# Kernel optimization log

Measured on AMD Instinct MI355X. Metric: run time of the kernel, lower is better.

## Reference

```python
import jax, jax.numpy as jnp
import numpy as np

N_HEAD = 12
TOP_M = 16
MIN_SIZE = 2
MAX_SIZE = 8
ALPHA = 1.0
EPS = 1e-6

# Note: in the torch source, minimize_det=True and minimize_det=False select the
# identical subset (the sign flip in the score is exactly undone by flipping the
# comparisons), so we implement the single equivalent rule: maximize
# s = -log(det(K_S K_S^T) + 1e-6) / |S|**alpha.

def _token(qi, i, k_all, v_all):
    """Greedy DPP subset selection for one query token i. qi:[d], k_all/v_all:[T,d]."""
    T, d = k_all.shape
    slots = jnp.arange(MAX_SIZE)
    sim = k_all @ qi
    sim = jnp.where(jnp.arange(T) <= i, sim, -jnp.inf)  # causal mask
    vals, topidx = jax.lax.top_k(sim, TOP_M)
    avail0 = jnp.isfinite(vals) & (topidx != i)  # i is removed from candidates
    k_cand = k_all[topidx]                        # [M,d]
    cand_norm = jnp.sum(k_cand * k_cand, axis=-1)  # [M]
    ki = k_all[i]
    sel0 = jnp.zeros((MAX_SIZE,), jnp.int32).at[0].set(i.astype(jnp.int32))
    s0 = jax.lax.stop_gradient(-jnp.log(jnp.dot(ki, ki) + EPS))  # |S|=1 => size^alpha=1

    def body(state, _):
        sel, count, cur_s, avail, done = state
        # E: selected key vectors in slots < count, zeros elsewhere
        E = jnp.where((slots < count)[:, None], k_all[sel], 0.0)  # [S,d]
        G0 = E @ E.T                                              # [S,S]
        cross = k_cand @ E.T  # [M,S]; column `count` is 0 since that E row is 0
        u = (slots == count).astype(E.dtype)  # one-hot insertion slot
        # Gram of S u {c} for every candidate c, identity-padded beyond slot count
        grams = (G0[None]
                 + u[None, :, None] * cross[:, None, :]
                 + cross[:, :, None] * u[None, None, :]
                 + cand_norm[:, None, None] * (u[:, None] * u[None, :])[None])
        grams = grams + jnp.diag(jnp.where(slots > count, 1.0, 0.0))[None]
        det = jnp.linalg.det(grams.astype(jnp.float32))  # [M]
        s = -jnp.log(det + EPS) / (count + 1).astype(jnp.float32) ** ALPHA
        s = jax.lax.stop_gradient(jnp.where(avail, s, -jnp.inf))
        best = jnp.argmax(s)
        best_s = s[best]
        accept = (~done) & jnp.any(avail) & ((best_s > cur_s) | (count < MIN_SIZE))
        sel = jnp.where(accept & (slots == count), topidx[best].astype(jnp.int32), sel)
        avail = avail & ~(accept & (jnp.arange(TOP_M) == best))
        cur_s = jnp.where(accept, best_s, cur_s)
        count = count + accept.astype(count.dtype)
        done = done | ~accept
        return (sel, count, cur_s, avail, done), None

    init = (sel0, jnp.int32(1), s0, avail0, jnp.bool_(False))
    (sel, count, _, _, _), _ = jax.lax.scan(body, init, None, length=MAX_SIZE - 1)
    w = (slots < count).astype(v_all.dtype)
    return (v_all[sel] * w[:, None]).sum(0) / count.astype(v_all.dtype)

_tokens = jax.vmap(_token, in_axes=(0, 0, None, None))  # over T

def _head(qh, kh, vh):
    return _tokens(qh, jnp.arange(qh.shape[0]), kh, vh)

_attn = jax.vmap(jax.vmap(_head))  # over B, H

def _forward(x, W_attn, b_attn, W_proj, b_proj):
    B, T, C = x.shape
    hs = C // N_HEAD
    qkv = x @ W_attn + b_attn
    q, k, v = jnp.split(qkv, 3, axis=-1)
    q = q.reshape(B, T, N_HEAD, hs).transpose(0, 2, 1, 3)
    k = k.reshape(B, T, N_HEAD, hs).transpose(0, 2, 1, 3)
    v = v.reshape(B, T, N_HEAD, hs).transpose(0, 2, 1, 3)
    y = _attn(q, k, v)  # [B,H,T,hs]
    y = y.transpose(0, 2, 1, 3).reshape(B, T, C)
    return y @ W_proj + b_proj  # dropout=0.0 (eval)

def setup_inputs():
    key = jax.random.key(0)
    ks = jax.random.split(key, 3)
    B, T, C = 4, 512, 768
    return {
        "x": jax.random.normal(ks[0], (B, T, C), jnp.float32),
        "W_attn": jax.random.normal(ks[1], (C, 3 * C), jnp.float32) * 0.02,
        "b_attn": jnp.zeros((3 * C,), jnp.float32),
        "W_proj": jax.random.normal(ks[2], (C, C), jnp.float32) * 0.02,
        "b_proj": jnp.zeros((C,), jnp.float32),
    }

def reference(x, W_attn, b_attn, W_proj, b_proj):
    return _forward(x, W_attn, b_attn, W_proj, b_proj)
```

## Files before the change

### kernel.cpp

```cpp
#include <hip/hip_runtime.h>
#include <math.h>

constexpr int Bc = 4, Tc = 512, Cc = 768, Hc = 12, HSc = 64;
constexpr int QKVN = 3 * Cc;
constexpr double EPSd = 1e-6;

typedef unsigned short u16;
typedef __attribute__((ext_vector_type(8))) short short8;
typedef __attribute__((ext_vector_type(4))) float f32x4;

__device__ __forceinline__ u16 f2bf(float x) {
  unsigned u = __float_as_uint(x);
  return (u16)((u + 0x7FFFu + ((u >> 16) & 1u)) >> 16);
}
__device__ __forceinline__ float bf2f(u16 h) {
  return __uint_as_float((unsigned)h << 16);
}

__device__ __forceinline__ void gload16(const u16* g, u16* l) {
  __builtin_amdgcn_global_load_lds(
      (const __attribute__((address_space(1))) void*)g,
      (__attribute__((address_space(3))) void*)l, 16, 0, 0);
}

__global__ void __launch_bounds__(256) convsplit3(
    const float* __restrict__ in, u16* __restrict__ H, u16* __restrict__ M,
    u16* __restrict__ L) {
  const int i = blockIdx.x * 256 + threadIdx.x;
  const float4 v = ((const float4*)in)[i];
  const float x[4] = {v.x, v.y, v.z, v.w};
  ushort4 hv, mv, lv;
  u16* hp = (u16*)&hv; u16* mp = (u16*)&mv; u16* lp = (u16*)&lv;
#pragma unroll
  for (int c = 0; c < 4; ++c) {
    const u16 h = f2bf(x[c]);
    const float r1 = x[c] - bf2f(h);
    const u16 m = f2bf(r1);
    const u16 l = f2bf(r1 - bf2f(m));
    hp[c] = h; mp[c] = m; lp[c] = l;
  }
  ((ushort4*)H)[i] = hv;
  ((ushort4*)M)[i] = mv;
  ((ushort4*)L)[i] = lv;
}

__global__ void __launch_bounds__(256) convsplit3_t(
    const float* __restrict__ W, u16* __restrict__ Th, u16* __restrict__ Tm,
    u16* __restrict__ Tl, int K, int Nn) {
  __shared__ float t[64][65];
  const int k0 = blockIdx.x * 64, n0 = blockIdx.y * 64;
#pragma unroll
  for (int u = 0; u < 16; ++u) {
    const int idx = u * 256 + threadIdx.x;
    const int r = idx >> 6, c = idx & 63;
    t[r][c] = W[(size_t)(k0 + r) * Nn + n0 + c];
  }
  __syncthreads();
#pragma unroll
  for (int u = 0; u < 16; ++u) {
    const int idx = u * 256 + threadIdx.x;
    const int n = idx >> 6, k = idx & 63;
    const float x = t[k][n];
    const u16 h = f2bf(x);
    const float r1 = x - bf2f(h);
    const u16 m = f2bf(r1);
    const u16 l = f2bf(r1 - bf2f(m));
    Th[(size_t)(n0 + n) * K + k0 + k] = h;
    Tm[(size_t)(n0 + n) * K + k0 + k] = m;
    Tl[(size_t)(n0 + n) * K + k0 + k] = l;
  }
}

template <bool WRITE_PARTIAL>
__global__ void __launch_bounds__(128, 2) gemm_mfma3(
    const u16* __restrict__ A, const u16* __restrict__ B,
    const float* __restrict__ bias, float* __restrict__ outp,
    int N, int kPerSplit, int strideA, int strideB) {
  __shared__ __align__(16) u16 AsF[3 * 64 * 32];
  __shared__ __align__(16) u16 BsF[3 * 128 * 32];
  const int tid = threadIdx.x;
  const int wid = tid >> 6;
  const int lane = tid & 63;
  const int lm = lane & 15, kg = lane >> 4;
  const int rb = blockIdx.x * 64;
  const int cb = blockIdx.y * 128;
  const int kBeg = blockIdx.z * kPerSplit;

  const int trow = tid >> 2;
  const int tc4 = tid & 3;
  const int krot = ((tc4 - (trow >> 1)) & 3) * 8;
  const int sLds = tid * 8;
  int aOff = (rb + trow) * 768 + kBeg + krot;
  int bOff = (cb + trow) * 768 + kBeg + krot;

  f32x4 acc[4][4];
#pragma unroll
  for (int mf = 0; mf < 4; ++mf)
#pragma unroll
    for (int nf = 0; nf < 4; ++nf) acc[mf][nf] = (f32x4){0.f, 0.f, 0.f, 0.f};

  const int nIter = kPerSplit / 32;
  const int ckA = ((kg + (lm >> 1)) & 3) * 8;

  for (int it = 0; it < nIter; ++it) {
    __syncthreads();
#pragma unroll
    for (int v = 0; v < 12; ++v)
      gload16(B + (size_t)(v >> 2) * strideB + (v & 3) * (32 * 768) + bOff,
              &BsF[(v >> 2) * 4096 + (v & 3) * 1024 + sLds]);
#pragma unroll
    for (int u = 0; u < 6; ++u)
      gload16(A + (size_t)(u >> 1) * strideA + (u & 1) * (32 * 768) + aOff,
              &AsF[(u >> 1) * 2048 + (u & 1) * 1024 + sLds]);
    aOff += 32; bOff += 32;
    __syncthreads();
    short8 ah[4], am[4], al[4];
#pragma unroll
    for (int mf = 0; mf < 4; ++mf) {
      const int ro = (mf * 16 + lm) * 32 + ckA;
      ah[mf] = *(const short8*)&AsF[ro];
      am[mf] = *(const short8*)&AsF[2048 + ro];
      al[mf] = *(const short8*)&AsF[4096 + ro];
    }
#pragma unroll
    for (int nf = 0; nf < 4; ++nf) {
      const int co = (wid * 64 + nf * 16 + lm) * 32 + ckA;
      const short8 bh = *(const short8*)&BsF[co];
      const short8 bm = *(const short8*)&BsF[4096 + co];
      const short8 bl = *(const short8*)&BsF[8192 + co];
#pragma unroll
      for (int mf = 0; mf < 4; ++mf) {
        acc[mf][nf] = __builtin_amdgcn_mfma_f32_16x16x32_bf16(
            al[mf], bh, acc[mf][nf], 0, 0, 0);
        acc[mf][nf] = __builtin_amdgcn_mfma_f32_16x16x32_bf16(
            ah[mf], bl, acc[mf][nf], 0, 0, 0);
        acc[mf][nf] = __builtin_amdgcn_mfma_f32_16x16x32_bf16(
            am[mf], bm, acc[mf][nf], 0, 0, 0);
        acc[mf][nf] = __builtin_amdgcn_mfma_f32_16x16x32_bf16(
            am[mf], bh, acc[mf][nf], 0, 0, 0);
        acc[mf][nf] = __builtin_amdgcn_mfma_f32_16x16x32_bf16(
            ah[mf], bm, acc[mf][nf], 0, 0, 0);
        acc[mf][nf] = __builtin_amdgcn_mfma_f32_16x16x32_bf16(
            ah[mf], bh, acc[mf][nf], 0, 0, 0);
      }
    }
  }

  const int colb = cb + wid * 64 + lm;
  if (WRITE_PARTIAL) {
    float* Pp = outp + (size_t)blockIdx.z * 2048 * N;
#pragma unroll
    for (int mf = 0; mf < 4; ++mf)
#pragma unroll
      for (int r2 = 0; r2 < 4; ++r2) {
        float* orow = Pp + (size_t)(rb + mf * 16 + kg * 4 + r2) * N + colb;
        orow[0]  = acc[mf][0][r2];
        orow[16] = acc[mf][1][r2];
        orow[32] = acc[mf][2][r2];
        orow[48] = acc[mf][3][r2];
      }
  } else {
    const float bb0 = bias[colb], bb1 = bias[colb + 16];
    const float bb2 = bias[colb + 32], bb3 = bias[colb + 48];
#pragma unroll
    for (int mf = 0; mf < 4; ++mf)
#pragma unroll
      for (int r2 = 0; r2 < 4; ++r2) {
        float* orow = outp + (size_t)(rb + mf * 16 + kg * 4 + r2) * N + colb;
        orow[0]  = acc[mf][0][r2] + bb0;
        orow[16] = acc[mf][1][r2] + bb1;
        orow[32] = acc[mf][2][r2] + bb2;
        orow[48] = acc[mf][3][r2] + bb3;
      }
  }
}

__global__ void __launch_bounds__(256) reduce_bias_kernel(
    const float* __restrict__ P, const float* __restrict__ bias,
    float* __restrict__ outp, int MN, int N, int KS) {
  const int idx4 = (blockIdx.x * 256 + threadIdx.x) * 4;
  float4 acc = *(const float4*)&P[idx4];
  for (int ks = 1; ks < KS; ++ks) {
    const float4 p = *(const float4*)&P[(size_t)ks * MN + idx4];
    acc.x += p.x; acc.y += p.y; acc.z += p.z; acc.w += p.w;
  }
  const int col = idx4 % N;
  const float4 b4 = *(const float4*)&bias[col];
  acc.x += b4.x; acc.y += b4.y; acc.z += b4.z; acc.w += b4.w;
  *(float4*)&outp[idx4] = acc;
}

__global__ void __launch_bounds__(256) sims_kernel(
    const float* __restrict__ qkv, float* __restrict__ S) {
  const int bh = blockIdx.y;
  const int b = bh / Hc, h = bh % Hc;
  int it = 0;
  {
    const int t = blockIdx.x;
    while ((it + 1) * (it + 2) / 2 <= t) ++it;
  }
  const int jt = blockIdx.x - it * (it + 1) / 2;
  const int tid = threadIdx.x;
  const int tx = tid & 15, ty = tid >> 4;
  __shared__ float Qs[HSc][68];
  __shared__ float Ks[HSc][68];
  const float* base = qkv + (size_t)b * Tc * QKVN + h * HSc;
  {
    const int row = tid >> 2;
    const int d0 = (tid & 3) * 16;
    const float* qrow = base + (size_t)(it * 64 + row) * QKVN;
    const float* krow = base + (size_t)(jt * 64 + row) * QKVN + Cc;
#pragma unroll
    for (int u = 0; u < 4; ++u) {
      const float4 q4 = *(const float4*)&qrow[d0 + u * 4];
      const float4 k4 = *(const float4*)&krow[d0 + u * 4];
      Qs[d0 + u * 4 + 0][row] = q4.x; Qs[d0 + u * 4 + 1][row] = q4.y;
      Qs[d0 + u * 4 + 2][row] = q4.z; Qs[d0 + u * 4 + 3][row] = q4.w;
      Ks[d0 + u * 4 + 0][row] = k4.x; Ks[d0 + u * 4 + 1][row] = k4.y;
      Ks[d0 + u * 4 + 2][row] = k4.z; Ks[d0 + u * 4 + 3][row] = k4.w;
    }
  }
  __syncthreads();
  float acc[4][4];
#pragma unroll
  for (int m = 0; m < 4; ++m)
#pragma unroll
    for (int n = 0; n < 4; ++n) acc[m][n] = 0.0f;
#pragma unroll 4
  for (int d = 0; d < HSc; ++d) {
    const float4 a4 = *(const float4*)&Qs[d][ty * 4];
    const float4 b4 = *(const float4*)&Ks[d][tx * 4];
    const float a[4] = {a4.x, a4.y, a4.z, a4.w};
    const float bv[4] = {b4.x, b4.y, b4.z, b4.w};
#pragma unroll
    for (int m = 0; m < 4; ++m)
#pragma unroll
      for (int n = 0; n < 4; ++n) acc[m][n] += a[m] * bv[n];
  }
  float* Shead = S + (size_t)bh * Tc * Tc;
#pragma unroll
  for (int m = 0; m < 4; ++m) {
    const int i = it * 64 + ty * 4 + m;
    float4 o4 = {acc[m][0], acc[m][1], acc[m][2], acc[m][3]};
    *(float4*)&Shead[(size_t)i * Tc + jt * 64 + tx * 4] = o4;
  }
}

__global__ void __launch_bounds__(256) topk_kernel(
    const float* __restrict__ S, int* __restrict__ topidx,
    unsigned* __restrict__ availB) {
  const int tid = threadIdx.x;
  const int wv = tid >> 6, lane = tid & 63;
  const int tok = blockIdx.x * 4 + wv;
  const int i = tok & (Tc - 1);
  const float4* Sq = reinterpret_cast<const float4*>(S + (size_t)tok * Tc);
  unsigned long long key[8];
#pragma unroll
  for (int r = 0; r < 2; ++r) {
    const float4 v4 = Sq[lane * 2 + r];
    const float vv[4] = {v4.x, v4.y, v4.z, v4.w};
#pragma unroll
    for (int c = 0; c < 4; ++c) {
      const int j = lane * 8 + r * 4 + c;
      const unsigned u = __float_as_uint(vv[c]);
      const unsigned s = (u & 0x80000000u) ? ~u : (u | 0x80000000u);
      key[r * 4 + c] = (j <= i)
          ? (((unsigned long long)s << 32) | (unsigned)(511 - j))
          : 0ull;
    }
  }
  unsigned avail = 0;
  for (int m = 0; m < 16; ++m) {
    unsigned long long bk = 0;
#pragma unroll
    for (int r = 0; r < 8; ++r) bk = (key[r] > bk) ? key[r] : bk;
#pragma unroll
    for (int msk = 1; msk <= 32; msk <<= 1) {
      const unsigned long long ok = __shfl_xor(bk, msk);
      bk = (ok > bk) ? ok : bk;
    }
    const int j = 511 - (int)(unsigned)(bk & 0xFFFFFFFFull);
    const unsigned shi = (unsigned)(bk >> 32);
    if (lane == 0) topidx[(size_t)tok * 16 + m] = j & 511;
    if (shi > 0x007FFFFFu && j != i) avail |= (1u << m);
#pragma unroll
    for (int r = 0; r < 8; ++r) key[r] = (key[r] == bk) ? 0ull : key[r];
  }
  if (lane == 0) availB[tok] = avail;
}

__global__ void __launch_bounds__(256, 4) select_kernel(
    const float* __restrict__ qkv, const int* __restrict__ topidx,
    const unsigned* __restrict__ availB, u16* __restrict__ yh,
    u16* __restrict__ ym, u16* __restrict__ yl) {
  const int tid = threadIdx.x;
  const int wv = tid >> 6, lane = tid & 63;
  const int half = lane >> 5;
  const int l32 = lane & 31;
  const int m = l32 >> 1;
  const int q = l32 & 1;
  const int hbase = half << 5;

  const int tok = blockIdx.x * 8 + wv * 2 + half;
  const int bh = tok >> 9;
  const int i = tok & (Tc - 1);
  const int b = bh / Hc;
  const int h = bh % Hc;

  const float* base = qkv + (size_t)b * Tc * QKVN + h * HSc;
  const float* kbase = base + Cc;
  const float* vbase = base + 2 * Cc;

  const int tidx = topidx[(size_t)tok * 16 + m];
  unsigned avail = availB[tok];

  float kreg[32], kireg[32];
  {
    const float* kc = kbase + (size_t)tidx * QKVN + q * 32;
    const float* ki = kbase + (size_t)i * QKVN + q * 32;
#pragma unroll
    for (int u = 0; u < 8; ++u) {
      const float4 c4 = *(const float4*)&kc[u * 4];
      const float4 i4 = *(const float4*)&ki[u * 4];
      kreg[u * 4 + 0] = c4.x; kreg[u * 4 + 1] = c4.y;
      kreg[u * 4 + 2] = c4.z; kreg[u * 4 + 3] = c4.w;
      kireg[u * 4 + 0] = i4.x; kireg[u * 4 + 1] = i4.y;
      kireg[u * 4 + 2] = i4.z; kireg[u * 4 + 3] = i4.w;
    }
  }
  float cnorm_f = 0.0f, c0_f = 0.0f, kii_f = 0.0f;
#pragma unroll
  for (int e = 0; e < 32; ++e) {
    cnorm_f += kreg[e] * kreg[e];
    c0_f += kreg[e] * kireg[e];
    kii_f += kireg[e] * kireg[e];
  }
  cnorm_f += __shfl_xor(cnorm_f, 1);
  c0_f += __shfl_xor(c0_f, 1);
  kii_f += __shfl_xor(kii_f, 1);

  const double kii = (double)kii_f;
  double z[8];
#pragma unroll
  for (int t = 0; t < 8; ++t) z[t] = 0.0;
  z[0] = (double)c0_f / sqrt(kii);
  double schur = (double)cnorm_f - z[0] * z[0];
  double detS = kii;
  double Dprev = 0.0;
  int count = 1;
  int sel[8];
  sel[0] = i;
#pragma unroll
  for (int a = 1; a < 8; ++a) sel[a] = 0;
  bool hdone = false;

#pragma unroll
  for (int it = 0; it < 7; ++it) {
    const double D = detS * schur + EPSd;
    const bool act = ((avail >> m) & 1u) != 0;
    const bool bad = !(D > 0.0);
    double dkey = act ? (bad ? -INFINITY : D) : INFINITY;
    int bm = m;
#pragma unroll
    for (int msk = 2; msk <= 16; msk <<= 1) {
      const double ok2 = __shfl_xor(dkey, msk);
      const int om = __shfl_xor(bm, msk);
      const bool t2 = (ok2 < dkey) || (ok2 == dkey && om < bm);
      dkey = t2 ? ok2 : dkey;
      bm = t2 ? om : bm;
    }
    const double Dbest = __shfl(D, hbase | (bm * 2));
    bool acc_ok;
    if (it == 0) {
      acc_ok = true;
    } else {
      double pA = Dbest, pB = Dprev;
#pragma unroll
      for (int j = 0; j < it; ++j) pA *= Dbest;
#pragma unroll
      for (int j = 0; j < it + 1; ++j) pB *= Dprev;
      acc_ok = ((avail >> bm) & 1u) && (Dbest >= 0.0) && (Dprev >= 0.0) &&
               (pA < pB);
    }
    const bool X = !hdone && (avail != 0u) && acc_ok;
    hdone = hdone || !X;
    if (X) {
      float cp_f = 0.0f;
#pragma unroll
      for (int e = 0; e < 32; ++e) {
        const float kb = __shfl(kreg[e], hbase | (bm * 2) | q);
        cp_f += kreg[e] * kb;
      }
      cp_f += __shfl_xor(cp_f, 1);
      const double schur_b = __shfl(schur, hbase | (bm * 2));
      double sum = 0.0;
#pragma unroll
      for (int t = 0; t <= it; ++t) {
        const double zbt = __shfl(z[t], hbase | (bm * 2));
        sum += z[t] * zbt;
      }
      const double znew = ((double)cp_f - sum) / sqrt(schur_b);
      z[it + 1] = znew;
      schur -= znew * znew;
      detS *= schur_b;
      Dprev = Dbest;
      avail &= ~(1u << bm);
      ++count;
      sel[it + 1] = __shfl(tidx, hbase | (bm * 2));
    }
    if (__all(hdone)) break;
  }

  double acc0 = 0.0, acc1 = 0.0;
#pragma unroll
  for (int a = 0; a < 8; ++a)
    if (a < count) {
      const float* vrow = vbase + (size_t)sel[a] * QKVN;
      acc0 += (double)vrow[l32];
      acc1 += (double)vrow[l32 + 32];
    }
  const float v0 = (float)(acc0 / (double)count);
  const float v1 = (float)(acc1 / (double)count);
  const size_t yidx = (((size_t)b * Tc + i) * Hc + h) * HSc + l32;
  {
    const u16 hv = f2bf(v0);
    const float r1 = v0 - bf2f(hv);
    const u16 mv = f2bf(r1);
    yh[yidx] = hv; ym[yidx] = mv; yl[yidx] = f2bf(r1 - bf2f(mv));
  }
  {
    const u16 hv = f2bf(v1);
    const float r1 = v1 - bf2f(hv);
    const u16 mv = f2bf(r1);
    yh[yidx + 32] = hv; ym[yidx + 32] = mv;
    yl[yidx + 32] = f2bf(r1 - bf2f(mv));
  }
}

extern "C" void kernel_launch(void* const* d_in, const int* in_sizes, int n_in,
                              void* d_out, int out_size, void* d_ws, size_t ws_size,
                              hipStream_t stream) {
  (void)in_sizes; (void)n_in; (void)out_size; (void)ws_size;
  const float* x  = (const float*)d_in[0];
  const float* Wa = (const float*)d_in[1];
  const float* ba = (const float*)d_in[2];
  const float* Wp = (const float*)d_in[3];
  const float* bp = (const float*)d_in[4];
  float* out = (float*)d_out;

  constexpr size_t XPLANE = (size_t)Bc * Tc * Cc;
  constexpr size_t WAPLANE = (size_t)QKVN * Cc;
  constexpr size_t WPPLANE = (size_t)Cc * Cc;

  float* qkv = (float*)d_ws;
  int* topidx = (int*)(qkv + (size_t)Bc * Tc * QKVN);
  unsigned* availB = (unsigned*)(topidx + (size_t)Bc * Hc * Tc * 16);
  float* regionB = (float*)(availB + (size_t)Bc * Hc * Tc);
  float* S = regionB;
  float* Pproj = regionB;
  u16* Xh = (u16*)regionB;
  u16* Wath = Xh + 3 * XPLANE;
  u16* Wpth = (u16*)(regionB + (size_t)3 * 2048 * Cc);
  u16* yhp = Wpth + 3 * WPPLANE;

  const int MNproj = Bc * Tc * Cc;

  hipLaunchKernelGGL(convsplit3, dim3(1536), dim3(256), 0, stream,
                     x, Xh, Xh + XPLANE, Xh + 2 * XPLANE);
  hipLaunchKernelGGL(convsplit3_t, dim3(12, 36), dim3(256), 0, stream,
                     Wa, Wath, Wath + WAPLANE, Wath + 2 * WAPLANE, Cc, QKVN);
  hipLaunchKernelGGL((gemm_mfma3<false>), dim3(32, QKVN / 128, 1), dim3(128),
                     0, stream, Xh, Wath, ba, qkv, QKVN, Cc,
                     (int)XPLANE, (int)WAPLANE);
  hipLaunchKernelGGL(sims_kernel, dim3(36, Bc * Hc), dim3(256), 0,
                     stream, qkv, S);
  hipLaunchKernelGGL(topk_kernel, dim3(Bc * Hc * Tc / 4), dim3(256), 0,
                     stream, S, topidx, availB);
  hipLaunchKernelGGL(select_kernel, dim3(Bc * Hc * Tc / 8), dim3(256), 0,
                     stream, qkv, topidx, availB,
                     yhp, yhp + XPLANE, yhp + 2 * XPLANE);
  hipLaunchKernelGGL(convsplit3_t, dim3(12, 12), dim3(256), 0, stream,
                     Wp, Wpth, Wpth + WPPLANE, Wpth + 2 * WPPLANE, Cc, Cc);
  hipLaunchKernelGGL((gemm_mfma3<true>), dim3(32, Cc / 128, 3), dim3(128), 0,
                     stream, yhp, Wpth, nullptr, Pproj, Cc, 256,
                     (int)XPLANE, (int)WPPLANE);
  hipLaunchKernelGGL(reduce_bias_kernel, dim3(MNproj / 1024), dim3(256), 0,
                     stream, Pproj, bp, out, MNproj, Cc, 3);
}
```

Measured before the change: 288.3 us.

## Double-buffer LDS tiles in split-bf16 MFMA GEMM to overlap loads with compute

The GEMM's shared-memory A/B tiles are doubled so the next k-slice is fetched with global_load_lds while the current slice feeds the MFMA chain. This removes one of the two barriers per k-step and aims to hide global-load latency behind matrix math. LDS use per block doubles, which may limit occupancy. The loop assumes an even iteration count: with an odd count the last compute(1) would read a stale buffer.

```diff
diff --git a/kernel.cpp b/kernel.cpp
--- a/kernel.cpp
+++ b/kernel.cpp
@@ -76,8 +76,8 @@
     const u16* __restrict__ A, const u16* __restrict__ B,
     const float* __restrict__ bias, float* __restrict__ outp,
     int N, int kPerSplit, int strideA, int strideB) {
-  __shared__ __align__(16) u16 AsF[3 * 64 * 32];
-  __shared__ __align__(16) u16 BsF[3 * 128 * 32];
+  __shared__ __align__(16) u16 AsF[2][3 * 64 * 32];
+  __shared__ __align__(16) u16 BsF[2][3 * 128 * 32];
   const int tid = threadIdx.x;
   const int wid = tid >> 6;
   const int lane = tid & 63;
@@ -102,32 +102,32 @@
   const int nIter = kPerSplit / 32;
   const int ckA = ((kg + (lm >> 1)) & 3) * 8;
 
-  for (int it = 0; it < nIter; ++it) {
-    __syncthreads();
+  auto stage = [&](int buf) {
 #pragma unroll
     for (int v = 0; v < 12; ++v)
       gload16(B + (size_t)(v >> 2) * strideB + (v & 3) * (32 * 768) + bOff,
-              &BsF[(v >> 2) * 4096 + (v & 3) * 1024 + sLds]);
+              &BsF[buf][(v >> 2) * 4096 + (v & 3) * 1024 + sLds]);
 #pragma unroll
     for (int u = 0; u < 6; ++u)
       gload16(A + (size_t)(u >> 1) * strideA + (u & 1) * (32 * 768) + aOff,
-              &AsF[(u >> 1) * 2048 + (u & 1) * 1024 + sLds]);
+              &AsF[buf][(u >> 1) * 2048 + (u & 1) * 1024 + sLds]);
     aOff += 32; bOff += 32;
-    __syncthreads();
+  };
+  auto compute = [&](int buf) {
     short8 ah[4], am[4], al[4];
 #pragma unroll
     for (int mf = 0; mf < 4; ++mf) {
       const int ro = (mf * 16 + lm) * 32 + ckA;
-      ah[mf] = *(const short8*)&AsF[ro];
-      am[mf] = *(const short8*)&AsF[2048 + ro];
-      al[mf] = *(const short8*)&AsF[4096 + ro];
+      ah[mf] = *(const short8*)&AsF[buf][ro];
+      am[mf] = *(const short8*)&AsF[buf][2048 + ro];
+      al[mf] = *(const short8*)&AsF[buf][4096 + ro];
     }
 #pragma unroll
     for (int nf = 0; nf < 4; ++nf) {
       const int co = (wid * 64 + nf * 16 + lm) * 32 + ckA;
-      const short8 bh = *(const short8*)&BsF[co];
-      const short8 bm = *(const short8*)&BsF[4096 + co];
-      const short8 bl = *(const short8*)&BsF[8192 + co];
+      const short8 bh = *(const short8*)&BsF[buf][co];
+      const short8 bm = *(const short8*)&BsF[buf][4096 + co];
+      const short8 bl = *(const short8*)&BsF[buf][8192 + co];
 #pragma unroll
       for (int mf = 0; mf < 4; ++mf) {
         acc[mf][nf] = __builtin_amdgcn_mfma_f32_16x16x32_bf16(
@@ -144,6 +144,17 @@
             ah[mf], bh, acc[mf][nf], 0, 0, 0);
       }
     }
+  };
+
+  stage(0);
+  __syncthreads();
+  for (int it = 0; it < nIter; it += 2) {
+    if (it + 1 < nIter) stage(1);
+    compute(0);
+    __syncthreads();
+    if (it + 2 < nIter) stage(0);
+    compute(1);
+    __syncthreads();
   }
 
   const int colb = cb + wid * 64 + lm;
```

After: 317.9 us. +10.3%, slower.
